# Kernel tuning notes

Measured on AMD Instinct MI355X. Metric: run time of the kernel, lower is better.

## Reference

```python
import jax, jax.numpy as jnp
import numpy as np

S = 1024; VOCAB = 100000; EMB = 300
POS_SZ = 64; CHAR_E = 50; CHAR_ENC = 128; WLEN = 16
NCHARS = 100; NPOSTAG = 50; NPOSITIONS = 1024
D = EMB + 3 * POS_SZ + CHAR_ENC  # word_rep_size = 620
BIH = 128   # per-direction LSTM hidden (bilstm_hidden_size // 2)
TLH = 256; LCC = 128; GCC = 256
NET = 8; NTAGS = 16; NREL = 16
TOKF = 2 * BIH + LCC + TLH       # 640
SENTF = 2 * TOKF + GCC           # 1536

def _p(k, shape):
    return 0.02 * jax.random.normal(k, shape, dtype=jnp.float32)

def setup_inputs():
    key = jax.random.key(0)
    ks = jax.random.split(key, 30)
    return {
        'word_inputs': jax.random.randint(ks[0], (1, S), 0, VOCAB),
        'char_inputs': jax.random.randint(ks[1], (1, S, WLEN), 0, NCHARS),
        'postag_inputs': jax.random.randint(ks[2], (1, S), 0, NPOSTAG),
        'dependency_inputs': jax.random.randint(ks[3], (1, S), 0, 64),
        'position_inputs': jax.random.randint(ks[4], (1, S), 0, NPOSITIONS),
        'topo_order': jnp.arange(S),  # children-before-parents order
        'parent': jnp.concatenate([jnp.arange(1, S), jnp.array([S])]),  # chain dep tree; root -> dummy slot S
        'pointed_token_idx': 5,
        'word_table': _p(ks[5], (VOCAB, EMB)),
        'char_table': _p(ks[6], (NCHARS, CHAR_E)),
        'char_conv_w': _p(ks[7], (CHAR_ENC, CHAR_E, 3)),
        'char_conv_b': jnp.zeros((CHAR_ENC,), jnp.float32),
        'postag_table': _p(ks[8], (NPOSTAG, POS_SZ)),
        'position_table': _p(ks[9], (NPOSITIONS, POS_SZ)),
        'lstm_f_Wx': _p(ks[10], (D, 4 * BIH)),
        'lstm_f_Wh': _p(ks[11], (BIH, 4 * BIH)),
        'lstm_f_b': jnp.zeros((4 * BIH,), jnp.float32),
        'lstm_b_Wx': _p(ks[12], (D, 4 * BIH)),
        'lstm_b_Wh': _p(ks[13], (BIH, 4 * BIH)),
        'lstm_b_b': jnp.zeros((4 * BIH,), jnp.float32),
        'word_cnn_w': _p(ks[14], (LCC, D, 3)),
        'word_cnn_b': jnp.zeros((LCC,), jnp.float32),
        'tl_Wiou': _p(ks[15], (D, 3 * TLH)),
        'tl_Uiou': _p(ks[16], (TLH, 3 * TLH)),
        'tl_biou': jnp.zeros((3 * TLH,), jnp.float32),
        'tl_Wf': _p(ks[17], (D, TLH)),
        'tl_Uf': _p(ks[18], (TLH, TLH)),
        'tl_bf': jnp.zeros((TLH,), jnp.float32),
        'sent_cnn_w': _p(ks[19], (GCC, D, 3)),
        'sent_cnn_b': jnp.zeros((GCC,), jnp.float32),
        'et_w': _p(ks[20], (GCC + TOKF, NET)),
        'et_b': jnp.zeros((NET,), jnp.float32),
        'crf_w': _p(ks[21], (SENTF, NTAGS)),
        'crf_b': jnp.zeros((NTAGS,), jnp.float32),
        'crf_trans': _p(ks[22], (NTAGS, NTAGS)),
        'rel_w': _p(ks[23], (SENTF, NREL)),
        'rel_b': jnp.zeros((NREL,), jnp.float32),
    }

def _conv1d(x, w, b):
    # x: [N, Cin, W], w: [Cout, Cin, K], padding=1 (matches nn.Conv1d(..., padding=1))
    y = jax.lax.conv_general_dilated(x, w, (1,), [(1, 1)], dimension_numbers=('NCW', 'OIW', 'NCW'))
    return y + b[None, :, None]

def _lstm(xs, Wx, Wh, b):
    H = Wh.shape[0]
    def step(carry, x):
        h, c = carry
        g = x @ Wx + h @ Wh + b
        i, f, gg, o = jnp.split(g, 4, axis=-1)
        c = jax.nn.sigmoid(f) * c + jax.nn.sigmoid(i) * jnp.tanh(gg)
        h = jax.nn.sigmoid(o) * jnp.tanh(c)
        return (h, c), h
    init = (jnp.zeros((H,), xs.dtype), jnp.zeros((H,), xs.dtype))
    _, hs = jax.lax.scan(step, init, xs)
    return hs

def _tree_lstm(x, order, parent, Wiou, Uiou, biou, Wf, Uf, bf):
    # ChildSum TreeLSTM over the whole dependency tree in topological order.
    # Equivalent to the source's per-token subtree recursion: each node's h
    # only depends on its subtree.
    Sn, H = x.shape[0], Uf.shape[0]
    xiou = x @ Wiou + biou                 # [S, 3H]
    xf = jnp.concatenate([x @ Wf + bf, jnp.zeros((1, H), x.dtype)], axis=0)  # dummy row for root's parent
    def step(carry, j):
        h, hsum, fcsum = carry
        iou = xiou[j] + hsum[j] @ Uiou
        i, o, u = jnp.split(iou, 3)
        cj = jax.nn.sigmoid(i) * jnp.tanh(u) + fcsum[j]
        hj = jax.nn.sigmoid(o) * jnp.tanh(cj)
        p = parent[j]
        f = jax.nn.sigmoid(xf[p] + hj @ Uf)  # per-child forget gate
        return (h.at[j].set(hj), hsum.at[p].add(hj), fcsum.at[p].add(f * cj)), None
    h0 = jnp.zeros((Sn, H), x.dtype)
    acc0 = jnp.zeros((Sn + 1, H), x.dtype)
    (h, _, _), _ = jax.lax.scan(step, (h0, acc0, acc0), order)
    return h

def _viterbi(emissions, trans):
    # emissions: [S, T]; trans[i, j] = score(i -> j)
    def step(score, e):
        s = score[:, None] + trans
        return jnp.max(s, axis=0) + e, jnp.argmax(s, axis=0)
    final, ptrs = jax.lax.scan(step, emissions[0], emissions[1:])
    last = jnp.argmax(final)
    def bt(tag, p):
        prev = p[tag]
        return prev, prev
    _, prevs = jax.lax.scan(bt, last, ptrs, reverse=True)
    return jnp.concatenate([prevs, last[None]])

def reference(word_inputs, char_inputs, postag_inputs, dependency_inputs, position_inputs, topo_order, parent, pointed_token_idx, word_table, char_table, char_conv_w, char_conv_b, postag_table, position_table, lstm_f_Wx, lstm_f_Wh, lstm_f_b, lstm_b_Wx, lstm_b_Wh, lstm_b_b, word_cnn_w, word_cnn_b, tl_Wiou, tl_Uiou, tl_biou, tl_Wf, tl_Uf, tl_bf, sent_cnn_w, sent_cnn_b, et_w, et_b, crf_w, crf_b, crf_trans, rel_w, rel_b):
    we = word_table[word_inputs]                                   # [1,S,EMB]
    cx = jnp.transpose(char_table[char_inputs[0]], (0, 2, 1))      # [S,CHAR_E,WLEN]
    ce = jnp.max(jax.nn.relu(_conv1d(cx, char_conv_w, char_conv_b)), axis=-1)[None]  # CharCNN -> [1,S,CHAR_ENC]
    pe = postag_table[postag_inputs]
    poe = position_table[position_inputs]
    de = position_table[dependency_inputs]                         # faithful to source bug: uses position table
    inputs = jnp.concatenate([we, ce, pe, poe, de], axis=-1)       # [1,S,D]
    x = inputs[0]
    hf = _lstm(x, lstm_f_Wx, lstm_f_Wh, lstm_f_b)
    hb = _lstm(x[::-1], lstm_b_Wx, lstm_b_Wh, lstm_b_b)[::-1]
    bilstm = jnp.concatenate([hf, hb], axis=-1)[None]              # [1,S,2*BIH]
    xc = jnp.transpose(inputs, (0, 2, 1))                          # [1,D,S]
    local_cnn = jnp.transpose(_conv1d(xc, word_cnn_w, word_cnn_b), (0, 2, 1))
    tree_h = _tree_lstm(x, topo_order, parent, tl_Wiou, tl_Uiou, tl_biou, tl_Wf, tl_Uf, tl_bf)[None]
    global_cnn = jnp.transpose(jnp.max(_conv1d(xc, sent_cnn_w, sent_cnn_b), axis=-1, keepdims=True), (0, 2, 1))  # [1,1,GCC]
    tokens_info = jnp.concatenate([bilstm, local_cnn, tree_h], axis=-1)  # [1,S,TOKF]
    ptr = tokens_info[:, pointed_token_idx, :]                     # [1,TOKF]
    ptr_info = jnp.broadcast_to(ptr[:, None, :], (1, S, TOKF))
    glob_info = jnp.broadcast_to(global_cnn, (1, S, GCC))
    sentence_encoding = jnp.concatenate([tokens_info, ptr_info, glob_info], axis=-1)  # dropout = identity (eval)
    one_vec = jnp.concatenate([global_cnn[:, 0, :], ptr], axis=-1)
    entitytype = jax.nn.softmax(one_vec @ et_w + et_b, axis=-1)
    entities = _viterbi(sentence_encoding[0] @ crf_w + crf_b, crf_trans)
    relations = jax.nn.sigmoid(sentence_encoding @ rel_w + rel_b)
    return sentence_encoding, entitytype, entities, relations
```

## Files before the change

### kernel.cpp

```cpp
#include <hip/hip_runtime.h>
#include <math.h>

#define SEQ   1024
#define DX    620
#define BIH   128
#define TLH   256
#define NTAGS 16

#define O_X      0
#define O_XGF    634880
#define O_XGB    (O_XGF + 524288)
#define O_XIOU   (O_XGB + 524288)
#define O_XF     (O_XIOU + 786432)
#define O_LCNN   (O_XF + 262400)
#define O_SCNN   (O_LCNN + 131072)
#define O_PART   (O_SCNN + 262144)
#define O_GCNN   (O_PART + 4096)
#define O_HF     (O_GCNN + 256)
#define O_HB     (O_HF + 131072)
#define O_TREEH  (O_HB + 131072)
#define O_IOUA   (O_TREEH + 262144)
#define O_FCSUM  (O_IOUA + 787200)
#define O_EMIS   (O_FCSUM + 262400)

#define SENT 0xFFFFFFFFu

typedef float f32x4_t __attribute__((ext_vector_type(4)));

__device__ __forceinline__ float sig_f(float x){ return 1.0f/(1.0f + __expf(-x)); }
__device__ __forceinline__ float tanh_f(float x){
  float ax = fabsf(x);
  float e  = __expf(-2.0f*ax);
  float t  = (1.0f - e)/(1.0f + e);
  return x < 0.0f ? -t : t;
}
__device__ __forceinline__ int physslot(int s){ return s ^ ((s>>3)&7); }

__global__ __launch_bounds__(128) void k_embed(
    const int* __restrict__ wi, const int* __restrict__ ci,
    const int* __restrict__ postag_in, const int* __restrict__ dep_in, const int* __restrict__ pos_in,
    const float* __restrict__ word_table, const float* __restrict__ char_table,
    const float* __restrict__ ccw, const float* __restrict__ ccb,
    const float* __restrict__ postag_table, const float* __restrict__ position_table,
    float* __restrict__ x)
{
  int s = blockIdx.x;
  int tid = threadIdx.x;
  __shared__ __align__(16) float ce[50][16];
  for (int idx = tid; idx < 800; idx += 128){
    int e = idx >> 4, t = idx & 15;
    ce[e][t] = char_table[ci[s*16 + t]*50 + e];
  }
  __syncthreads();
  float* xr = x + (size_t)s*DX;
  const float* wrow = word_table + (size_t)wi[s]*300;
  for (int d = tid; d < 300; d += 128) xr[d] = wrow[d];
  {
    int oc = tid;
    const float* wp = ccw + oc*150;
    float acc[16];
    float b = ccb[oc];
    #pragma unroll
    for (int t=0;t<16;t++) acc[t] = b;
    for (int ic=0; ic<50; ic++){
      float w0 = wp[ic*3+0], w1 = wp[ic*3+1], w2 = wp[ic*3+2];
      float cv[16];
      float4 c0 = *(const float4*)&ce[ic][0];
      float4 c1 = *(const float4*)&ce[ic][4];
      float4 c2 = *(const float4*)&ce[ic][8];
      float4 c3 = *(const float4*)&ce[ic][12];
      cv[0]=c0.x;cv[1]=c0.y;cv[2]=c0.z;cv[3]=c0.w;
      cv[4]=c1.x;cv[5]=c1.y;cv[6]=c1.z;cv[7]=c1.w;
      cv[8]=c2.x;cv[9]=c2.y;cv[10]=c2.z;cv[11]=c2.w;
      cv[12]=c3.x;cv[13]=c3.y;cv[14]=c3.z;cv[15]=c3.w;
      #pragma unroll
      for (int t=0;t<16;t++){
        float a = cv[t]*w1;
        if (t > 0)  a += cv[t-1]*w0;
        if (t < 15) a += cv[t+1]*w2;
        acc[t] += a;
      }
    }
    float m = acc[0];
    #pragma unroll
    for (int t=1;t<16;t++) m = fmaxf(m, acc[t]);
    xr[300 + oc] = fmaxf(m, 0.0f);
  }
  if (tid < 64){
    int d = tid;
    xr[428 + d] = postag_table[postag_in[s]*64 + d];
    xr[492 + d] = position_table[pos_in[s]*64 + d];
    xr[556 + d] = position_table[dep_in[s]*64 + d];
  }
}

struct GemmArgs {
  const float* B[6];
  const float* bias[6];
  float*       C[6];
  int N[6]; int K[6]; int amode[6];
};

__global__ __launch_bounds__(256) void k_gemm(const float* __restrict__ x, GemmArgs ga)
{
  int z = blockIdx.z;
  int N = ga.N[z], K = ga.K[z], amode = ga.amode[z];
  int bn = blockIdx.x*64;
  if (bn >= N) return;
  int bm = blockIdx.y*64;
  const float* __restrict__ Bm = ga.B[z];
  __shared__ __align__(16) float As[20][64];
  __shared__ __align__(16) float Bs[20][64];
  int tid = threadIdx.x;
  int lane = tid & 63, kg = tid >> 6;
  int tx = tid & 15, ty = tid >> 4;
  float acc[4][4] = {{0.f}};
  for (int k0 = 0; k0 < K; k0 += 20){
    #pragma unroll
    for (int kk=0; kk<5; kk++){
      int k = kg*5 + kk;
      float av;
      if (amode == 0){
        av = x[(size_t)(bm+lane)*DX + k0 + k];
      } else {
        int kc = k0 + k;
        int d  = kc/3;
        int sh = kc - d*3 - 1;
        int row = bm + lane + sh;
        av = (row >= 0 && row < SEQ) ? x[(size_t)row*DX + d] : 0.0f;
      }
      As[k][lane] = av;
      Bs[k][lane] = (amode==0) ? Bm[(size_t)(k0+k)*N + bn + lane]
                               : Bm[(size_t)(bn+lane)*K + k0 + k];
    }
    __syncthreads();
    #pragma unroll
    for (int k=0;k<20;k++){
      float4 a = *(const float4*)&As[k][ty<<2];
      float4 b = *(const float4*)&Bs[k][tx<<2];
      acc[0][0]+=a.x*b.x; acc[0][1]+=a.x*b.y; acc[0][2]+=a.x*b.z; acc[0][3]+=a.x*b.w;
      acc[1][0]+=a.y*b.x; acc[1][1]+=a.y*b.y; acc[1][2]+=a.y*b.z; acc[1][3]+=a.y*b.w;
      acc[2][0]+=a.z*b.x; acc[2][1]+=a.z*b.y; acc[2][2]+=a.z*b.z; acc[2][3]+=a.z*b.w;
      acc[3][0]+=a.w*b.x; acc[3][1]+=a.w*b.y; acc[3][2]+=a.w*b.z; acc[3][3]+=a.w*b.w;
    }
    __syncthreads();
  }
  const float* bias = ga.bias[z];
  float* C = ga.C[z];
  float4 bb;
  bb.x = bias[bn+(tx<<2)+0]; bb.y = bias[bn+(tx<<2)+1];
  bb.z = bias[bn+(tx<<2)+2]; bb.w = bias[bn+(tx<<2)+3];
  #pragma unroll
  for (int i=0;i<4;i++){
    int row = bm + (ty<<2) + i;
    float4 o;
    o.x = acc[i][0] + bb.x; o.y = acc[i][1] + bb.y;
    o.z = acc[i][2] + bb.z; o.w = acc[i][3] + bb.w;
    *(float4*)&C[(size_t)row*N + bn + (tx<<2)] = o;
  }
}

__global__ __launch_bounds__(256) void k_gmax(const float* __restrict__ scnn, float* __restrict__ gcnn){
  int c = threadIdx.x;
  float m = -3.0e38f;
  #pragma unroll 8
  for (int s = 0; s < SEQ; s++) m = fmaxf(m, scnn[(size_t)s*256 + c]);
  gcnn[c] = m;
}

__global__ __launch_bounds__(256, 1) void k_recur(
    const float* __restrict__ xg_f, const float* __restrict__ xg_b,
    const float* __restrict__ Wh_f, const float* __restrict__ Wh_b,
    const float* __restrict__ xiou, const float* __restrict__ xf,
    const float* __restrict__ Uiou, const float* __restrict__ Uf,
    const int* __restrict__ order, const int* __restrict__ parent,
    float* __restrict__ hf, float* __restrict__ hb,
    float* tree_h, float* iou_acc, float* fcsum)
{
  int blk = blockIdx.x;
  int tid = threadIdx.x;

  if (blk >= 4){
    const float* xg  = (blk == 4) ? xg_f : xg_b;
    const float* Wh  = (blk == 4) ? Wh_f : Wh_b;
    float* hout      = (blk == 4) ? hf : hb;
    int cg = tid >> 1, rg = tid & 1;
    float4 w[4][16];
    #pragma unroll
    for (int cc=0;cc<4;cc++){
      int col = cg*4 + cc;
      #pragma unroll
      for (int r4=0;r4<16;r4++){
        int row = rg*64 + r4*4;
        w[cc][r4].x = Wh[(size_t)(row+0)*512 + col];
        w[cc][r4].y = Wh[(size_t)(row+1)*512 + col];
        w[cc][r4].z = Wh[(size_t)(row+2)*512 + col];
        w[cc][r4].w = Wh[(size_t)(row+3)*512 + col];
      }
    }
    #pragma unroll
    for (int cc=0;cc<4;cc++)
      #pragma unroll
      for (int r4=0;r4<16;r4++)
        asm volatile("" : "+v"(w[cc][r4].x), "+v"(w[cc][r4].y), "+v"(w[cc][r4].z), "+v"(w[cc][r4].w));

    __shared__ __align__(16) float lhl[BIH];
    __shared__ float lcst[BIH];
    __shared__ float gl[512];
    if (tid < BIH){ lhl[tid] = 0.f; lcst[tid] = 0.f; }
    __syncthreads();
    const float4* lhl4 = (const float4*)lhl;
    for (int st=0; st<SEQ; st++){
      int n = (blk == 4) ? st : (SEQ-1-st);
      float4 xg4 = make_float4(0.f,0.f,0.f,0.f);
      if (rg == 0) xg4 = *(const float4*)&xg[(size_t)n*512 + cg*4];
      float acc[4] = {0.f,0.f,0.f,0.f};
      #pragma unroll
      for (int r4=0;r4<16;r4++){
        float4 h4 = lhl4[rg*16 + r4];
        #pragma unroll
        for (int cc=0;cc<4;cc++)
          acc[cc] += h4.x*w[cc][r4].x + h4.y*w[cc][r4].y + h4.z*w[cc][r4].z + h4.w*w[cc][r4].w;
      }
      #pragma unroll
      for (int cc=0;cc<4;cc++) acc[cc] += __shfl_xor(acc[cc], 1);
      if (rg == 0){
        float4 o = make_float4(acc[0]+xg4.x, acc[1]+xg4.y, acc[2]+xg4.z, acc[3]+xg4.w);
        *(float4*)&gl[cg*4] = o;
      }
      __syncthreads();
      if (tid < BIH){
        float gi = gl[tid], gf = gl[BIH+tid], gg = gl[2*BIH+tid], go = gl[3*BIH+tid];
        float c = sig_f(gf)*lcst[tid] + sig_f(gi)*tanh_f(gg);
        float h = sig_f(go)*tanh_f(c);
        lcst[tid] = c;
        lhl[tid] = h;
        hout[(size_t)n*BIH + tid] = h;
      }
      __syncthreads();
    }
    return;
  }

  int cg = tid >> 3, rg = tid & 7;
  int ulo = blk*64;
  float4 w[8][8];
  #pragma unroll
  for (int cc=0;cc<8;cc++){
    int c = cg*8 + cc;
    const float* Wsrc; size_t stride; int gcol;
    if (c < 192){ Wsrc = Uiou; stride = 768; gcol = (c>>6)*TLH + ulo + (c&63); }
    else        { Wsrc = Uf;   stride = 256; gcol = ulo + (c-192); }
    #pragma unroll
    for (int r4=0;r4<8;r4++){
      int row = rg*32 + r4*4;
      w[cc][r4].x = Wsrc[(size_t)(row+0)*stride + gcol];
      w[cc][r4].y = Wsrc[(size_t)(row+1)*stride + gcol];
      w[cc][r4].z = Wsrc[(size_t)(row+2)*stride + gcol];
      w[cc][r4].w = Wsrc[(size_t)(row+3)*stride + gcol];
    }
  }
  #pragma unroll
  for (int cc=0;cc<8;cc++)
    #pragma unroll
    for (int r4=0;r4<8;r4++)
      asm volatile("" : "+v"(w[cc][r4].x), "+v"(w[cc][r4].y), "+v"(w[cc][r4].z), "+v"(w[cc][r4].w));

  __shared__ __align__(16) float hl[TLH];
  __shared__ float colsum[TLH];
  __shared__ float cprev[64];
  __shared__ int ord_l[SEQ];
  __shared__ int par_l[SEQ];
  for (int i=tid; i<SEQ; i+=256){ ord_l[i] = order[i]; par_l[i] = parent[i]; }
  __syncthreads();
  const float4* hl4 = (const float4*)hl;

  for (int t=0; t<SEQ; t++){
    int n  = ord_l[t];
    int m  = (t > 0) ? ord_l[t-1] : 0;
    int pp = (t > 0) ? par_l[m] : -1;
    bool ppeq = (pp == n);

    float xi=0.f, xo=0.f, xu=0.f, ac_i=0.f, ac_o=0.f, ac_u=0.f, fcn=0.f;
    float xfv=0.f, po_i=0.f, po_o=0.f, po_u=0.f, po_f=0.f;
    if (tid < 64){
      int uu = ulo + tid;
      xi   = xiou[(size_t)n*768 + uu];
      xo   = xiou[(size_t)n*768 + 256 + uu];
      xu   = xiou[(size_t)n*768 + 512 + uu];
      ac_i = iou_acc[(size_t)n*768 + uu];
      ac_o = iou_acc[(size_t)n*768 + 256 + uu];
      ac_u = iou_acc[(size_t)n*768 + 512 + uu];
      fcn  = fcsum[(size_t)n*256 + uu];
      if (t > 0){
        xfv = xf[(size_t)pp*256 + uu];
        if (!ppeq){
          po_i = iou_acc[(size_t)pp*768 + uu];
          po_o = iou_acc[(size_t)pp*768 + 256 + uu];
          po_u = iou_acc[(size_t)pp*768 + 512 + uu];
          po_f = fcsum[(size_t)pp*256 + uu];
        }
      }
    }

    if (t > 0){
      float acc[8] = {0.f,0.f,0.f,0.f,0.f,0.f,0.f,0.f};
      int base = rg << 3;
      #pragma unroll
      for (int r4=0;r4<8;r4++){
        float4 h4 = hl4[base + (r4 ^ rg)];
        #pragma unroll
        for (int cc=0;cc<8;cc++)
          acc[cc] += h4.x*w[cc][r4].x + h4.y*w[cc][r4].y + h4.z*w[cc][r4].z + h4.w*w[cc][r4].w;
      }
      #pragma unroll
      for (int cc=0;cc<8;cc++){
        acc[cc] += __shfl_xor(acc[cc], 1);
        acc[cc] += __shfl_xor(acc[cc], 2);
        acc[cc] += __shfl_xor(acc[cc], 4);
      }
      if (rg == 0){
        *(float4*)&colsum[cg*8]     = make_float4(acc[0], acc[1], acc[2], acc[3]);
        *(float4*)&colsum[cg*8 + 4] = make_float4(acc[4], acc[5], acc[6], acc[7]);
      }
    }
    __syncthreads();

    if (tid < 64){
      int uu = ulo + tid;
      float ai = ac_i, ao = ac_o, au = ac_u, fcs = fcn;
      if (t > 0){
        float vi = colsum[tid], vo = colsum[64+tid], vuu = colsum[128+tid], vf = colsum[192+tid];
        float fg  = sig_f(xfv + vf);
        float fcc = fg * cprev[tid];
        if (ppeq){
          ai += vi; ao += vo; au += vuu; fcs += fcc;
        } else {
          iou_acc[(size_t)pp*768 + uu]       = po_i + vi;
          iou_acc[(size_t)pp*768 + 256 + uu] = po_o + vo;
          iou_acc[(size_t)pp*768 + 512 + uu] = po_u + vuu;
          fcsum[(size_t)pp*256 + uu]         = po_f + fcc;
        }
      }
      float cc = sig_f(xi + ai)*tanh_f(xu + au) + fcs;
      float hh = sig_f(xo + ao)*tanh_f(cc);
      cprev[tid] = cc;
      int s = uu >> 2;
      hl[physslot(s)*4 + (uu & 3)] = hh;
      float* tp = &tree_h[(size_t)n*TLH + uu];
      asm volatile("global_store_dword %0, %1, off sc0 sc1" :: "v"(tp), "v"(hh) : "memory");
    } else if (tid < 112){
      int p  = tid - 64;
      int qi = (p < (ulo >> 2)) ? p : p + 16;
      const float* tp = tree_h + (size_t)n*TLH + qi*4;
      const unsigned* up = (const unsigned*)tp;
      union { f32x4_t v; float4 f; unsigned u[4]; } pol;
      int spins = 0;
      while (true){
        asm volatile("global_load_dwordx4 %0, %1, off sc0 sc1\n\ts_waitcnt vmcnt(0)"
                     : "=v"(pol.v) : "v"(tp) : "memory");
        if ((pol.u[0] != SENT) & (pol.u[1] != SENT) & (pol.u[2] != SENT) & (pol.u[3] != SENT)) break;
        if (++spins > 64){
          pol.u[0] = __hip_atomic_load(up+0, __ATOMIC_RELAXED, __HIP_MEMORY_SCOPE_AGENT);
          pol.u[1] = __hip_atomic_load(up+1, __ATOMIC_RELAXED, __HIP_MEMORY_SCOPE_AGENT);
          pol.u[2] = __hip_atomic_load(up+2, __ATOMIC_RELAXED, __HIP_MEMORY_SCOPE_AGENT);
          pol.u[3] = __hip_atomic_load(up+3, __ATOMIC_RELAXED, __HIP_MEMORY_SCOPE_AGENT);
          if ((pol.u[0] != SENT) & (pol.u[1] != SENT) & (pol.u[2] != SENT) & (pol.u[3] != SENT)) break;
          spins = 0;
        }
      }
      *(float4*)&hl[physslot(qi)*4] = pol.f;
    }
    __syncthreads();
  }
}

__global__ __launch_bounds__(256) void k_assemble(
    const float* __restrict__ hf, const float* __restrict__ hb,
    const float* __restrict__ lcnn, const float* __restrict__ tree_h,
    const float* __restrict__ gcnn,
    const float* __restrict__ crf_w, const float* __restrict__ crf_b,
    const float* __restrict__ rel_w, const float* __restrict__ rel_b,
    const int* __restrict__ ptk,
    float* __restrict__ se_out, float* __restrict__ emis, float* __restrict__ rel_out)
{
  int s = blockIdx.x, tid = threadIdx.x;
  int p = ptk[0];
  __shared__ float se[1536];
  for (int d = tid; d < 1536; d += 256){
    float v;
    if      (d < 128)  v = hf[(size_t)s*128 + d];
    else if (d < 256)  v = hb[(size_t)s*128 + d-128];
    else if (d < 384)  v = lcnn[(size_t)s*128 + d-256];
    else if (d < 640)  v = tree_h[(size_t)s*256 + d-384];
    else if (d < 768)  v = hf[(size_t)p*128 + d-640];
    else if (d < 896)  v = hb[(size_t)p*128 + d-768];
    else if (d < 1024) v = lcnn[(size_t)p*128 + d-896];
    else if (d < 1280) v = tree_h[(size_t)p*256 + d-1024];
    else               v = gcnn[d-1280];
    se[d] = v;
    se_out[(size_t)s*1536 + d] = v;
  }
  __syncthreads();
  int o = tid >> 3, l = tid & 7;
  const float* W = (o < 16) ? crf_w : rel_w;
  int oc = (o < 16) ? o : (o - 16);
  float a = 0.f;
  for (int k = l; k < 1536; k += 8) a += se[k]*W[(size_t)k*16 + oc];
  for (int off = 4; off; off >>= 1) a += __shfl_down(a, off, 8);
  if (l == 0){
    if (o < 16) emis[(size_t)s*16 + o] = a + crf_b[o];
    else        rel_out[(size_t)s*16 + oc] = sig_f(a + rel_b[oc]);
  }
}

__global__ __launch_bounds__(256) void k_entity(
    const float* __restrict__ hf, const float* __restrict__ hb,
    const float* __restrict__ lcnn, const float* __restrict__ tree_h,
    const float* __restrict__ gcnn,
    const float* __restrict__ et_w, const float* __restrict__ et_b,
    const int* __restrict__ ptk, float* __restrict__ out_et)
{
  __shared__ float ov[896];
  __shared__ float lg[8];
  int tid = threadIdx.x;
  int p = ptk[0];
  for (int d = tid; d < 896; d += 256){
    float v;
    if      (d < 256) v = gcnn[d];
    else if (d < 384) v = hf[(size_t)p*128 + d-256];
    else if (d < 512) v = hb[(size_t)p*128 + d-384];
    else if (d < 640) v = lcnn[(size_t)p*128 + d-512];
    else              v = tree_h[(size_t)p*256 + d-640];
    ov[d] = v;
  }
  __syncthreads();
  int o = tid >> 5, l = tid & 31;
  float a = 0.f;
  for (int k = l; k < 896; k += 32) a += ov[k]*et_w[(size_t)k*8 + o];
  for (int off = 16; off; off >>= 1) a += __shfl_down(a, off, 32);
  if (l == 0) lg[o] = a + et_b[o];
  __syncthreads();
  if (tid == 0){
    float mx = lg[0];
    for (int i=1;i<8;i++) mx = fmaxf(mx, lg[i]);
    float e[8], sum = 0.f;
    for (int i=0;i<8;i++){ e[i] = __expf(lg[i]-mx); sum += e[i]; }
    for (int i=0;i<8;i++) out_et[i] = e[i]/sum;
  }
}

__global__ __launch_bounds__(128) void k_viterbi(
    const float* __restrict__ emis, const float* __restrict__ trans, float* __restrict__ out_e)
{
  __shared__ float ring[64][16];
  __shared__ float sc[16], nsc[16];
  __shared__ float tr[256];
  __shared__ unsigned char ptrs[1023*16];
  int tid = threadIdx.x;
  for (int i=tid; i<256; i+=128) tr[i] = trans[i];
  for (int i=tid; i<33*16; i+=128) ring[i>>4][i&15] = emis[i];
  if (tid < 16) sc[tid] = emis[tid];
  __syncthreads();
  int j = (tid & 63) >> 2, iq = tid & 3;
  for (int t=1; t<1024; t++){
    if (tid >= 64){
      int lr = tid - 64;
      int tl = t + 32;
      if (lr < 16 && tl < 1024) ring[tl & 63][lr] = emis[(size_t)tl*16 + lr];
    } else {
      float best = -3.0e38f; int barg = 0;
      #pragma unroll
      for (int ii=0; ii<4; ii++){
        int i = iq*4 + ii;
        float v = sc[i] + tr[i*16 + j];
        if (v > best){ best = v; barg = i; }
      }
      #pragma unroll
      for (int off=1; off<4; off<<=1){
        float ovv = __shfl_down(best, off, 4);
        int   oaa = __shfl_down(barg, off, 4);
        if (ovv > best){ best = ovv; barg = oaa; }
      }
      if (iq == 0){
        nsc[j] = best + ring[t & 63][j];
        ptrs[(t-1)*16 + j] = (unsigned char)barg;
      }
    }
    __syncthreads();
    if (tid < 16) sc[tid] = nsc[tid];
    __syncthreads();
  }
  if (tid == 0){
    float b = sc[0]; int last = 0;
    #pragma unroll
    for (int i=1;i<16;i++){ if (sc[i] > b){ b = sc[i]; last = i; } }
    out_e[1023] = (float)last;
    int cur = last;
    for (int t=1022; t>=0; t--){ cur = (int)ptrs[t*16 + cur]; out_e[t] = (float)cur; }
  }
}

extern "C" void kernel_launch(void* const* d_in, const int* in_sizes, int n_in,
                              void* d_out, int out_size, void* d_ws, size_t ws_size,
                              hipStream_t stream)
{
  (void)in_sizes; (void)n_in; (void)out_size; (void)ws_size;
  const int*   wi         = (const int*)d_in[0];
  const int*   ci         = (const int*)d_in[1];
  const int*   postag_in  = (const int*)d_in[2];
  const int*   dep_in     = (const int*)d_in[3];
  const int*   pos_in     = (const int*)d_in[4];
  const int*   order      = (const int*)d_in[5];
  const int*   parent     = (const int*)d_in[6];
  const int*   ptk        = (const int*)d_in[7];
  const float* word_table = (const float*)d_in[8];
  const float* char_table = (const float*)d_in[9];
  const float* ccw        = (const float*)d_in[10];
  const float* ccb        = (const float*)d_in[11];
  const float* postag_tab = (const float*)d_in[12];
  const float* pos_tab    = (const float*)d_in[13];
  const float* Wx_f       = (const float*)d_in[14];
  const float* Wh_f       = (const float*)d_in[15];
  const float* b_f        = (const float*)d_in[16];
  const float* Wx_b       = (const float*)d_in[17];
  const float* Wh_b       = (const float*)d_in[18];
  const float* b_b        = (const float*)d_in[19];
  const float* wcnn_w     = (const float*)d_in[20];
  const float* wcnn_b     = (const float*)d_in[21];
  const float* Wiou       = (const float*)d_in[22];
  const float* Uiou       = (const float*)d_in[23];
  const float* biou       = (const float*)d_in[24];
  const float* Wf_t       = (const float*)d_in[25];
  const float* Uf_t       = (const float*)d_in[26];
  const float* bf_t       = (const float*)d_in[27];
  const float* scnn_w     = (const float*)d_in[28];
  const float* scnn_b     = (const float*)d_in[29];
  const float* et_w       = (const float*)d_in[30];
  const float* et_b       = (const float*)d_in[31];
  const float* crf_w      = (const float*)d_in[32];
  const float* crf_b      = (const float*)d_in[33];
  const float* crf_trans  = (const float*)d_in[34];
  const float* rel_w      = (const float*)d_in[35];
  const float* rel_b      = (const float*)d_in[36];

  float* ws = (float*)d_ws;
  float* x      = ws + O_X;
  float* xg_f   = ws + O_XGF;
  float* xg_b   = ws + O_XGB;
  float* xiou   = ws + O_XIOU;
  float* xf     = ws + O_XF;
  float* lcnn   = ws + O_LCNN;
  float* scnn   = ws + O_SCNN;
  float* gcnn   = ws + O_GCNN;
  float* hf     = ws + O_HF;
  float* hb     = ws + O_HB;
  float* tree_h = ws + O_TREEH;
  float* iou_acc= ws + O_IOUA;
  float* fcsum  = ws + O_FCSUM;
  float* emis   = ws + O_EMIS;

  float* outF     = (float*)d_out;
  float* se_out   = outF;
  float* et_out   = outF + 1572864;
  float* ent_out  = outF + 1572872;
  float* rel_out  = outF + 1573896;

  hipMemsetAsync(xf, 0, (size_t)1025*256*sizeof(float), stream);
  hipMemsetAsync(iou_acc, 0, ((size_t)1025*768 + 1025*256)*sizeof(float), stream);
  hipMemsetAsync(tree_h, 0xFF, (size_t)1024*256*sizeof(float), stream);

  k_embed<<<SEQ, 128, 0, stream>>>(wi, ci, postag_in, dep_in, pos_in,
                                   word_table, char_table, ccw, ccb,
                                   postag_tab, pos_tab, x);

  GemmArgs ga;
  ga.B[0]=Wx_f;  ga.bias[0]=b_f;   ga.C[0]=xg_f; ga.N[0]=512; ga.K[0]=620;  ga.amode[0]=0;
  ga.B[1]=Wx_b;  ga.bias[1]=b_b;   ga.C[1]=xg_b; ga.N[1]=512; ga.K[1]=620;  ga.amode[1]=0;
  ga.B[2]=Wiou;  ga.bias[2]=biou;  ga.C[2]=xiou; ga.N[2]=768; ga.K[2]=620;  ga.amode[2]=0;
  ga.B[3]=Wf_t;  ga.bias[3]=bf_t;  ga.C[3]=xf;   ga.N[3]=256; ga.K[3]=620;  ga.amode[3]=0;
  ga.B[4]=wcnn_w;ga.bias[4]=wcnn_b;ga.C[4]=lcnn; ga.N[4]=128; ga.K[4]=1860; ga.amode[4]=1;
  ga.B[5]=scnn_w;ga.bias[5]=scnn_b;ga.C[5]=scnn; ga.N[5]=256; ga.K[5]=1860; ga.amode[5]=1;
  k_gemm<<<dim3(12,16,6), 256, 0, stream>>>(x, ga);

  k_gmax<<<1, 256, 0, stream>>>(scnn, gcnn);

  k_recur<<<6, 256, 0, stream>>>(xg_f, xg_b, Wh_f, Wh_b, xiou, xf, Uiou, Uf_t,
                                 order, parent, hf, hb, tree_h, iou_acc, fcsum);

  k_assemble<<<SEQ, 256, 0, stream>>>(hf, hb, lcnn, tree_h, gcnn,
                                      crf_w, crf_b, rel_w, rel_b, ptk,
                                      se_out, emis, rel_out);

  k_entity<<<1, 256, 0, stream>>>(hf, hb, lcnn, tree_h, gcnn, et_w, et_b, ptk, et_out);

  k_viterbi<<<1, 128, 0, stream>>>(emis, crf_trans, ent_out);
}
```

Measured before the change: 3.279 ms.

## Place tree-LSTM blocks on one XCD and relax cross-block polling coherence

Launches 32 blocks and keeps only ids 0,8,16,24 for the four tree-LSTM workers plus ids 1 and 9 for the two BiLSTM directions. Round-robin dispatch would then put the four tree workers on the same XCD so they can share its L2. Cross-block handoff of tree_h now stores with sc0 before the sc0 sc1 store, and the poll reads with sc0 only, using the full sc0 sc1 load every fourth try. This replaces the atomic-load fallback and is meant to cut latency in the 1024-step serial exchange. It relies on the block-to-XCD mapping being round-robin, and on L2 coherence within an XCD, neither of which is guaranteed.

```diff
diff --git a/kernel.cpp b/kernel.cpp
--- a/kernel.cpp
+++ b/kernel.cpp
@@ -177,13 +177,18 @@
     float* __restrict__ hf, float* __restrict__ hb,
     float* tree_h, float* iou_acc, float* fcsum)
 {
-  int blk = blockIdx.x;
+  int bid = blockIdx.x;
   int tid = threadIdx.x;
-
-  if (blk >= 4){
-    const float* xg  = (blk == 4) ? xg_f : xg_b;
-    const float* Wh  = (blk == 4) ? Wh_f : Wh_b;
-    float* hout      = (blk == 4) ? hf : hb;
+  int role = -1;
+  if ((bid & 7) == 0 && bid < 32) role = bid >> 3;
+  else if (bid == 1) role = 4;
+  else if (bid == 9) role = 5;
+  if (role < 0) return;
+
+  if (role >= 4){
+    const float* xg  = (role == 4) ? xg_f : xg_b;
+    const float* Wh  = (role == 4) ? Wh_f : Wh_b;
+    float* hout      = (role == 4) ? hf : hb;
     int cg = tid >> 1, rg = tid & 1;
     float4 w[4][16];
     #pragma unroll
@@ -211,7 +216,7 @@
     __syncthreads();
     const float4* lhl4 = (const float4*)lhl;
     for (int st=0; st<SEQ; st++){
-      int n = (blk == 4) ? st : (SEQ-1-st);
+      int n = (role == 4) ? st : (SEQ-1-st);
       float4 xg4 = make_float4(0.f,0.f,0.f,0.f);
       if (rg == 0) xg4 = *(const float4*)&xg[(size_t)n*512 + cg*4];
       float acc[4] = {0.f,0.f,0.f,0.f};
@@ -242,6 +247,7 @@
     return;
   }
 
+  int blk = role;
   int cg = tid >> 3, rg = tid & 7;
   int ulo = blk*64;
   float4 w[8][8];
@@ -348,26 +354,23 @@
       int s = uu >> 2;
       hl[physslot(s)*4 + (uu & 3)] = hh;
       float* tp = &tree_h[(size_t)n*TLH + uu];
+      asm volatile("global_store_dword %0, %1, off sc0"     :: "v"(tp), "v"(hh) : "memory");
       asm volatile("global_store_dword %0, %1, off sc0 sc1" :: "v"(tp), "v"(hh) : "memory");
     } else if (tid < 112){
       int p  = tid - 64;
       int qi = (p < (ulo >> 2)) ? p : p + 16;
       const float* tp = tree_h + (size_t)n*TLH + qi*4;
-      const unsigned* up = (const unsigned*)tp;
       union { f32x4_t v; float4 f; unsigned u[4]; } pol;
-      int spins = 0;
+      unsigned kk = 0;
       while (true){
-        asm volatile("global_load_dwordx4 %0, %1, off sc0 sc1\n\ts_waitcnt vmcnt(0)"
-                     : "=v"(pol.v) : "v"(tp) : "memory");
+        if ((kk & 3u) == 3u)
+          asm volatile("global_load_dwordx4 %0, %1, off sc0 sc1\n\ts_waitcnt vmcnt(0)"
+                       : "=v"(pol.v) : "v"(tp) : "memory");
+        else
+          asm volatile("global_load_dwordx4 %0, %1, off sc0\n\ts_waitcnt vmcnt(0)"
+                       : "=v"(pol.v) : "v"(tp) : "memory");
+        kk++;
         if ((pol.u[0] != SENT) & (pol.u[1] != SENT) & (pol.u[2] != SENT) & (pol.u[3] != SENT)) break;
-        if (++spins > 64){
-          pol.u[0] = __hip_atomic_load(up+0, __ATOMIC_RELAXED, __HIP_MEMORY_SCOPE_AGENT);
-          pol.u[1] = __hip_atomic_load(up+1, __ATOMIC_RELAXED, __HIP_MEMORY_SCOPE_AGENT);
-          pol.u[2] = __hip_atomic_load(up+2, __ATOMIC_RELAXED, __HIP_MEMORY_SCOPE_AGENT);
-          pol.u[3] = __hip_atomic_load(up+3, __ATOMIC_RELAXED, __HIP_MEMORY_SCOPE_AGENT);
-          if ((pol.u[0] != SENT) & (pol.u[1] != SENT) & (pol.u[2] != SENT) & (pol.u[3] != SENT)) break;
-          spins = 0;
-        }
       }
       *(float4*)&hl[physslot(qi)*4] = pol.f;
     }
@@ -585,8 +588,8 @@
 
   k_gmax<<<1, 256, 0, stream>>>(scnn, gcnn);
 
-  k_recur<<<6, 256, 0, stream>>>(xg_f, xg_b, Wh_f, Wh_b, xiou, xf, Uiou, Uf_t,
-                                 order, parent, hf, hb, tree_h, iou_acc, fcsum);
+  k_recur<<<32, 256, 0, stream>>>(xg_f, xg_b, Wh_f, Wh_b, xiou, xf, Uiou, Uf_t,
+                                  order, parent, hf, hb, tree_h, iou_acc, fcsum);
 
   k_assemble<<<SEQ, 256, 0, stream>>>(hf, hb, lcnn, tree_h, gcnn,
                                       crf_w, crf_b, rel_w, rel_b, ptk,
```

Measured after the change: 3.264 ms. No clear change (-0.4%).
